# Performance work log

Hardware: AMD Instinct MI355X
Metric: run time of the kernel (lower is better)

Reference implementation:

```python
import jax, jax.numpy as jnp
import numpy as np

B, D, H, O, E, K = 8192, 1024, 4096, 1024, 8, 2

def setup_inputs() -> dict:
    key = jax.random.key(0)
    ks = jax.random.split(key, 8)
    x = jax.random.normal(ks[0], (B, D), dtype=jnp.float32)
    topk_idx = jax.random.randint(ks[1], (B, K), 0, E, dtype=jnp.int32)
    weights = jax.random.uniform(ks[2], (B, K), dtype=jnp.float32)
    s1 = 1.0 / np.sqrt(D)
    s2 = 1.0 / np.sqrt(H)
    W1 = jax.random.uniform(ks[3], (E, D, H), minval=-s1, maxval=s1, dtype=jnp.float32)
    b1 = jax.random.uniform(ks[4], (E, H), minval=-s1, maxval=s1, dtype=jnp.float32)
    W2 = jax.random.uniform(ks[5], (E, H, O), minval=-s2, maxval=s2, dtype=jnp.float32)
    b2 = jax.random.uniform(ks[6], (E, O), minval=-s2, maxval=s2, dtype=jnp.float32)
    return {"x": x, "topk_idx": topk_idx, "weights": weights,
            "W1": W1, "b1": b1, "W2": W2, "b2": b2}

def reference(x, topk_idx, weights, W1, b1, W2, b2):
    # Per-token gate mass for each expert: gate[b,e] = sum_i weights[b,i]*[topk_idx[b,i]==e]
    # Equivalent to the original masked gather/scatter combine (duplicates in topk_idx sum).
    out = jnp.zeros((x.shape[0], W2.shape[-1]), dtype=x.dtype)
    for e in range(W1.shape[0]):  # small fixed loop over experts
        gate_e = jnp.sum(weights * (topk_idx == e), axis=1)  # [B]
        h = jax.nn.relu(x @ W1[e] + b1[e])                   # [B,H]
        out_e = h @ W2[e] + b2[e]                            # [B,O]
        out = out + gate_e[:, None] * out_e
    return out
```

## Files before the change

kernel.cpp:

```cpp
#include <hip/hip_runtime.h>
#include <stdint.h>

#define B_TOK 8192
#define D_DIM 1024
#define H_DIM 4096
#define O_DIM 1024
#define E_NUM 8
#define K_TOP 2
#define NPAIR (B_TOK * K_TOP)

typedef short bf16x8 __attribute__((ext_vector_type(8)));
typedef float f32x4 __attribute__((ext_vector_type(4)));

struct Hdr {
    int counts[8];
    int offsets[9];
    int cursor[8];
    int total1, total2;
    int base1[9];
    int base2[9];
};

__device__ __forceinline__ unsigned short f2bf(float f) {
    union { float f; unsigned int u; } v; v.f = f;
    unsigned int u = v.u;
    unsigned int r = (u + 0x7fffu + ((u >> 16) & 1u)) >> 16;
    return (unsigned short)r;
}

__device__ __forceinline__ float bf2f(unsigned short s) {
    union { unsigned int u; float f; } v;
    v.u = ((unsigned int)s) << 16;
    return v.f;
}

__device__ __forceinline__ void async16(const void* g, const void* l) {
    __builtin_amdgcn_global_load_lds(
        (__attribute__((address_space(1))) void*)(uintptr_t)g,
        (__attribute__((address_space(3))) void*)(uint32_t)(uintptr_t)l,
        16, 0, 0);
}


__global__ void cvt_x_kernel(const float* __restrict__ x, unsigned short* __restrict__ xb) {
    int i = (blockIdx.x * 256 + threadIdx.x) * 4;
    float4 v = *(const float4*)(x + i);
    ushort4 o;
    o.x = f2bf(v.x); o.y = f2bf(v.y); o.z = f2bf(v.z); o.w = f2bf(v.w);
    *(ushort4*)(xb + i) = o;
}

__global__ __launch_bounds__(256) void tconv_kernel(const float* __restrict__ in,
                                                    unsigned short* __restrict__ out,
                                                    int R, int C) {
    __shared__ float t[64 * 69];
    int e = blockIdx.z;
    const float* ip = in + (size_t)e * R * C;
    unsigned short* op = out + (size_t)e * R * C;
    int c0 = blockIdx.x * 64, r0 = blockIdx.y * 64;
    int tid = threadIdx.x;
    int lr = tid >> 4;
    int lc = (tid & 15) * 4;
#pragma unroll
    for (int i = 0; i < 4; i++) {
        int row = lr + i * 16;
        float4 v = *(const float4*)&ip[(size_t)(r0 + row) * C + c0 + lc];
        t[row * 69 + lc + 0] = v.x;
        t[row * 69 + lc + 1] = v.y;
        t[row * 69 + lc + 2] = v.z;
        t[row * 69 + lc + 3] = v.w;
    }
    __syncthreads();
#pragma unroll
    for (int i = 0; i < 4; i++) {
        int c = lr + i * 16;
        ushort4 o;
        o.x = f2bf(t[(lc + 0) * 69 + c]);
        o.y = f2bf(t[(lc + 1) * 69 + c]);
        o.z = f2bf(t[(lc + 2) * 69 + c]);
        o.w = f2bf(t[(lc + 3) * 69 + c]);
        *(ushort4*)&op[(size_t)(c0 + c) * R + r0 + lc] = o;
    }
}


__global__ void route_count_kernel(const int* __restrict__ topk, Hdr* hdr) {
    __shared__ int cnt[8];
    int tid = threadIdx.x;
    if (tid < 8) cnt[tid] = 0;
    __syncthreads();
    for (int i = tid; i < NPAIR; i += 1024) atomicAdd(&cnt[topk[i]], 1);
    __syncthreads();
    if (tid == 0) {
        int off = 0, t1 = 0, t2 = 0;
        for (int e = 0; e < 8; e++) {
            int c = cnt[e];
            hdr->counts[e] = c;
            hdr->offsets[e] = off;
            hdr->cursor[e] = off;
            hdr->base1[e] = t1;
            hdr->base2[e] = t2;
            int mt1 = (c + 255) >> 8;
            int mt2 = (c + 127) >> 7;
            t1 += mt1 * (H_DIM / 256);
            t2 += mt2 * (O_DIM / 128);
            off += c;
        }
        hdr->offsets[8] = off;
        hdr->base1[8] = t1;
        hdr->base2[8] = t2;
        hdr->total1 = t1;
        hdr->total2 = t2;
    }
}

__global__ void route_fill_kernel(const int* __restrict__ topk, const float* __restrict__ wts,
                                  Hdr* hdr, int* __restrict__ ptok, float* __restrict__ pgate,
                                  int* __restrict__ pslot) {
    int i = blockIdx.x * 256 + threadIdx.x;
    int e = topk[i];
    int pos = atomicAdd(&hdr->cursor[e], 1);
    ptok[pos] = i >> 1;
    pgate[pos] = wts[i];
    pslot[i] = pos;
}

__global__ void ws_fail_kernel(float* out) { out[0] = 1.0e9f; }


#define ASL(BUF, KH) ((BUF) * 32768 + (KH) * 16384)

#define STG_A(BUF, KH, KOFF) do { \
    async16(Ab + srcA[0] + (KOFF), smem + ASL(BUF, KH) + wu * 2048); \
    async16(Ab + srcA[1] + (KOFF), smem + ASL(BUF, KH) + wu * 2048 + 1024); } while (0)

#define STG_B(BUF, KH, KOFF) do { \
    async16(Bb + srcB[0] + (KOFF), smem + 65536 + ASL(BUF, KH) + wu * 2048); \
    async16(Bb + srcB[1] + (KOFF), smem + 65536 + ASL(BUF, KH) + wu * 2048 + 1024); } while (0)

#define VM6 asm volatile("s_waitcnt vmcnt(6)" ::: "memory")
#define VM0 asm volatile("s_waitcnt vmcnt(0)" ::: "memory")
#define NOPX ((void)0)

#define PHASE0(BUF, KH, STAGE, CKPT) do { \
    STAGE; \
    bq[0] = *(const bf16x8*)&smem[pBo[0] + ASL(BUF, KH)]; \
    bq[1] = *(const bf16x8*)&smem[pBo[1] + ASL(BUF, KH)]; \
    bq[2] = *(const bf16x8*)&smem[pBo[2] + ASL(BUF, KH)]; \
    bq[3] = *(const bf16x8*)&smem[pBo[3] + ASL(BUF, KH)]; \
    aq[0] = *(const bf16x8*)&smem[pAo[0] + ASL(BUF, KH)]; \
    aq[1] = *(const bf16x8*)&smem[pAo[1] + ASL(BUF, KH)]; \
    aq[2] = *(const bf16x8*)&smem[pAo[2] + ASL(BUF, KH)]; \
    aq[3] = *(const bf16x8*)&smem[pAo[3] + ASL(BUF, KH)]; \
    __builtin_amdgcn_s_barrier(); \
    asm volatile("s_waitcnt lgkmcnt(0)" ::: "memory"); \
    __builtin_amdgcn_s_setprio(1); \
    _Pragma("unroll") \
    for (int q_ = 0; q_ < 4; ++q_) { \
        _Pragma("unroll") \
        for (int n_ = 0; n_ < 4; ++n_) \
            acc[q_][n_] = __builtin_amdgcn_mfma_f32_16x16x32_bf16(aq[q_], bq[n_], acc[q_][n_], 0, 0, 0); \
    } \
    __builtin_amdgcn_s_setprio(0); \
    CKPT; \
    __builtin_amdgcn_s_barrier(); \
} while (0)

#define PHASE1(BUF, KH, STAGE, CKPT) do { \
    STAGE; \
    aq[0] = *(const bf16x8*)&smem[pAo[4] + ASL(BUF, KH)]; \
    aq[1] = *(const bf16x8*)&smem[pAo[5] + ASL(BUF, KH)]; \
    aq[2] = *(const bf16x8*)&smem[pAo[6] + ASL(BUF, KH)]; \
    aq[3] = *(const bf16x8*)&smem[pAo[7] + ASL(BUF, KH)]; \
    __builtin_amdgcn_s_barrier(); \
    asm volatile("s_waitcnt lgkmcnt(0)" ::: "memory"); \
    __builtin_amdgcn_s_setprio(1); \
    _Pragma("unroll") \
    for (int q_ = 0; q_ < 4; ++q_) { \
        _Pragma("unroll") \
        for (int n_ = 0; n_ < 4; ++n_) \
            acc[4 + q_][n_] = __builtin_amdgcn_mfma_f32_16x16x32_bf16(aq[q_], bq[n_], acc[4 + q_][n_], 0, 0, 0); \
    } \
    __builtin_amdgcn_s_setprio(0); \
    CKPT; \
    __builtin_amdgcn_s_barrier(); \
} while (0)

template <int KD, int N, bool GATHER>
__global__ __launch_bounds__(512, 2) void moe_gemm256_kernel(
    const unsigned short* __restrict__ A,
    const unsigned short* __restrict__ Bt,
    const float* __restrict__ bias,
    const Hdr* __restrict__ hdr,
    const int* __restrict__ ptok,
    unsigned short* __restrict__ outp) {

    extern __shared__ __align__(16) char smem[];
    constexpr int NT = KD / 64;
    constexpr int NI = NT / 2;
    static_assert(NT >= 4 && (NT % 2) == 0, "K-tile count");

    const int tid = threadIdx.x;
    const int lane = tid & 63;
    const int wv = tid >> 6;
    const int wu = __builtin_amdgcn_readfirstlane(wv);
    const int lr = lane & 15;
    const int lkg = lane >> 4;
    const int wr = wv >> 2;
    const int wc = wv & 3;

    const int total = hdr->total1;
    const int* tb = hdr->base1;

    int chunk = (total + 7) >> 3;
    int seq = (blockIdx.x & 7) * chunk + (blockIdx.x >> 3);
    if (seq >= total) return;

    int e = 0;
#pragma unroll
    for (int j = 1; j < 8; j++)
        if (seq >= tb[j]) e = j;
    e = __builtin_amdgcn_readfirstlane(e);
    int lt = seq - tb[e];
    int cnt = hdr->counts[e], off = hdr->offsets[e];
    int MT = (cnt + 255) >> 8;
    int mtile = lt % MT, ntile = lt / MT;
    int m0 = mtile * 256, n0 = ntile * 256;

    const char* Ab = (const char*)A;
    const char* Bb = (const char*)(Bt + (size_t)e * ((size_t)N * KD));

    uint32_t srcA[2], srcB[2];
#pragma unroll
    for (int l = 0; l < 2; ++l) {
        int g = wv * 128 + l * 64 + lane;
        int rp = g >> 2, cp = g & 3;
        int c = (cp - (rp >> 1)) & 3;
        int q = off + m0 + rp;
        q = q > NPAIR - 1 ? NPAIR - 1 : q;
        uint32_t rowA = GATHER ? (uint32_t)ptok[q] : (uint32_t)q;
        srcA[l] = rowA * (uint32_t)(KD * 2) + (uint32_t)(c * 16);
        srcB[l] = (uint32_t)(n0 + rp) * (uint32_t)(KD * 2) + (uint32_t)(c * 16);
    }

    uint32_t pAo[8], pBo[4];
#pragma unroll
    for (int mr = 0; mr < 8; ++mr) {
        int r = wr * 128 + mr * 16 + lr;
        pAo[mr] = (uint32_t)(r * 64 + ((lkg + (r >> 1)) & 3) * 16);
    }
#pragma unroll
    for (int nr = 0; nr < 4; ++nr) {
        int r = wc * 64 + nr * 16 + lr;
        pBo[nr] = (uint32_t)(65536 + r * 64 + ((lkg + (r >> 1)) & 3) * 16);
    }

    f32x4 acc[8][4];
#pragma unroll
    for (int i = 0; i < 8; ++i)
#pragma unroll
        for (int j = 0; j < 4; ++j)
            acc[i][j] = (f32x4){0.f, 0.f, 0.f, 0.f};
    bf16x8 aq[4], bq[4];

    STG_A(0, 0, 0u);   STG_B(0, 0, 0u);
    STG_A(0, 1, 64u);  STG_B(0, 1, 64u);
    STG_A(1, 0, 128u); STG_B(1, 0, 128u);
    STG_B(1, 1, 192u);
    VM0;
    __builtin_amdgcn_s_barrier();

    for (int it = 0; it < NI - 1; ++it) {
        const uint32_t kb = (uint32_t)it * 256u;
        PHASE0(0, 0, STG_A(1, 1, kb + 192u), NOPX);
        PHASE1(0, 0, STG_B(0, 0, kb + 256u), NOPX);
        PHASE0(0, 1, STG_A(0, 0, kb + 256u), NOPX);
        PHASE1(0, 1, STG_B(0, 1, kb + 320u), VM6);
        PHASE0(1, 0, STG_A(0, 1, kb + 320u), NOPX);
        PHASE1(1, 0, STG_B(1, 0, kb + 384u), NOPX);
        PHASE0(1, 1, STG_A(1, 0, kb + 384u), NOPX);
        PHASE1(1, 1, STG_B(1, 1, kb + 448u), VM6);
    }
    {
        const uint32_t kb = (uint32_t)(NI - 1) * 256u;
        PHASE0(0, 0, STG_A(1, 1, kb + 192u), NOPX);
        PHASE1(0, 0, NOPX, NOPX);
        PHASE0(0, 1, NOPX, NOPX);
        PHASE1(0, 1, NOPX, VM0);
        PHASE0(1, 0, NOPX, NOPX);
        PHASE1(1, 0, NOPX, NOPX);
        PHASE0(1, 1, NOPX, NOPX);
        PHASE1(1, 1, NOPX, NOPX);
    }

    unsigned short* eb = (unsigned short*)smem;
    int rows_valid = cnt - m0;
    if (rows_valid > 256) rows_valid = 256;
#pragma unroll
    for (int pass = 0; pass < 2; ++pass) {
        __syncthreads();
        if (wr == pass) {
#pragma unroll
            for (int nr = 0; nr < 4; ++nr) {
                int n = wc * 64 + nr * 16 + lr;
                float bv = bias[(size_t)e * N + n0 + n];
#pragma unroll
                for (int mr = 0; mr < 8; ++mr) {
#pragma unroll
                    for (int r2 = 0; r2 < 4; ++r2) {
                        int ml = mr * 16 + lkg * 4 + r2;
                        float v = acc[mr][nr][r2] + bv;
                        if (GATHER) v = v > 0.f ? v : 0.f;
                        eb[ml * 264 + n] = f2bf(v);
                    }
                }
            }
        }
        __syncthreads();
        int rv = rows_valid - pass * 128;
        if (rv > 128) rv = 128;
#pragma unroll
        for (int j = 0; j < 8; ++j) {
            int idx = j * 512 + tid;
            int row = idx >> 5;
            int c16 = idx & 31;
            if (row < rv) {
                uint4 v = *(const uint4*)&eb[row * 264 + c16 * 8];
                *(uint4*)&outp[(size_t)(off + m0 + pass * 128 + row) * N + n0 + c16 * 8] = v;
            }
        }
    }
}

template <int K, int N, bool GATHER>
__global__ __launch_bounds__(256, 4) void moe_gemm128_kernel(
    const unsigned short* __restrict__ A,
    const unsigned short* __restrict__ Bt,
    const float* __restrict__ bias,
    const Hdr* __restrict__ hdr,
    const int* __restrict__ ptok,
    unsigned short* __restrict__ outp) {

    __shared__ __align__(16) unsigned short smem[128 * 132];
    unsigned short* As = smem;
    unsigned short* Bs = smem + 128 * 64;

    const int tid = threadIdx.x;
    const int lane = tid & 63;
    const int wv = tid >> 6;
    const int wu = __builtin_amdgcn_readfirstlane(wv);
    const int wm = (wv & 1) * 64;
    const int wn = (wv >> 1) * 64;
    const int lr = lane & 15;
    const int lkg = lane >> 4;

    const int total = hdr->total2;
    const int* tb = hdr->base2;
    constexpr int NT = N / 128;

    int chunk = (total + 7) >> 3;
    int seq = (blockIdx.x & 7) * chunk + (blockIdx.x >> 3);
    if (seq >= total) return;

    int e = 0;
#pragma unroll
    for (int j = 1; j < 8; j++)
        if (seq >= tb[j]) e = j;
    e = __builtin_amdgcn_readfirstlane(e);
    int lt = seq - tb[e];
    int cnt = hdr->counts[e], off = hdr->offsets[e];
    int MT = (cnt + 127) >> 7;

    int band = lt / (NT * 8);
    int r = lt - band * (NT * 8);
    int mrem = MT - band * 8;
    mrem = mrem > 8 ? 8 : mrem;
    int gsz = mrem * 8;
    int g = r / gsz;
    int rg = r - g * gsz;
    int gm = rg % mrem;
    int gn = rg / mrem;
    int mtile = band * 8 + gm;
    int ntile = g * 8 + gn;
    int m0 = mtile * 128, n0 = ntile * 128;

    const char* Ab = (const char*)A;
    const char* Bb = (const char*)(Bt + (size_t)e * ((size_t)N * K));
    uint32_t offA[4], offB[4];
#pragma unroll
    for (int i = 0; i < 4; i++) {
        int s = i * 256 + tid;
        int rr = s >> 3;
        int cl = (s & 7) ^ (rr & 7);
        int p = off + m0 + rr;
        p = p > NPAIR - 1 ? NPAIR - 1 : p;
        uint32_t row = GATHER ? (uint32_t)ptok[p] : (uint32_t)p;
        offA[i] = (row * (uint32_t)K + (uint32_t)cl * 8u) * 2u;
        offB[i] = (((uint32_t)(n0 + rr)) * (uint32_t)K + (uint32_t)cl * 8u) * 2u;
    }

    f32x4 zero = {0.f, 0.f, 0.f, 0.f};
    f32x4 acc[4][4];
#pragma unroll
    for (int mt = 0; mt < 4; mt++)
#pragma unroll
        for (int nt = 0; nt < 4; nt++) acc[mt][nt] = zero;

    for (int k0 = 0; k0 < K; k0 += 64) {
#pragma unroll
        for (int i = 0; i < 4; i++) {
            async16(Ab + offA[i], &As[(i * 256 + wu * 64) * 8]);
            async16(Bb + offB[i], &Bs[(i * 256 + wu * 64) * 8]);
            offA[i] += 128;
            offB[i] += 128;
        }
        __syncthreads();
#pragma unroll
        for (int ks = 0; ks < 2; ks++) {
            bf16x8 af[4];
#pragma unroll
            for (int q = 0; q < 4; q++) {
                int ra = wm + q * 16 + lr;
                int ca = (ks * 4 + lkg) ^ (ra & 7);
                af[q] = *(const bf16x8*)&As[ra * 64 + ca * 8];
            }
#pragma unroll
            for (int nt = 0; nt < 4; nt++) {
                int rb = wn + nt * 16 + lr;
                int cb = (ks * 4 + lkg) ^ (rb & 7);
                bf16x8 bfr = *(const bf16x8*)&Bs[rb * 64 + cb * 8];
#pragma unroll
                for (int mt = 0; mt < 4; mt++)
                    acc[mt][nt] = __builtin_amdgcn_mfma_f32_16x16x32_bf16(
                        af[mt], bfr, acc[mt][nt], 0, 0, 0);
            }
        }
        __syncthreads();
    }

#pragma unroll
    for (int nt = 0; nt < 4; nt++) {
        int n = wn + nt * 16 + lr;
        float bv = bias[(size_t)e * N + n0 + n];
#pragma unroll
        for (int mt = 0; mt < 4; mt++) {
#pragma unroll
            for (int r2 = 0; r2 < 4; r2++) {
                int m = wm + mt * 16 + lkg * 4 + r2;
                float v = acc[mt][nt][r2] + bv;
                if (GATHER) v = v > 0.f ? v : 0.f;
                smem[m * 132 + n] = f2bf(v);
            }
        }
    }
    __syncthreads();
    int rows_valid = cnt - m0;
    if (rows_valid > 128) rows_valid = 128;
#pragma unroll
    for (int j = 0; j < 16; j++) {
        int idx = j * 256 + tid;
        int row = idx >> 5;
        int lc8 = idx & 31;
        if (row < rows_valid) {
            uint2 v = *(const uint2*)&smem[row * 132 + lc8 * 4];
            *(uint2*)&outp[(size_t)(off + m0 + row) * N + n0 + lc8 * 4] = v;
        }
    }
}

__global__ void combine_kernel(const unsigned short* __restrict__ oslot,
                               const int* __restrict__ pslot,
                               const float* __restrict__ wts,
                               float* __restrict__ out) {
    int tok = blockIdx.x;
    int s0 = pslot[tok * 2], s1 = pslot[tok * 2 + 1];
    float g0 = wts[tok * 2], g1 = wts[tok * 2 + 1];
    int n = threadIdx.x * 4;
    ushort4 a = *(const ushort4*)&oslot[(size_t)s0 * O_DIM + n];
    ushort4 b = *(const ushort4*)&oslot[(size_t)s1 * O_DIM + n];
    float4 o;
    o.x = g0 * bf2f(a.x) + g1 * bf2f(b.x);
    o.y = g0 * bf2f(a.y) + g1 * bf2f(b.y);
    o.z = g0 * bf2f(a.z) + g1 * bf2f(b.z);
    o.w = g0 * bf2f(a.w) + g1 * bf2f(b.w);
    *(float4*)&out[(size_t)tok * O_DIM + n] = o;
}


extern "C" void kernel_launch(void* const* d_in, const int* in_sizes, int n_in,
                              void* d_out, int out_size, void* d_ws, size_t ws_size,
                              hipStream_t stream) {
    const float* x   = (const float*)d_in[0];
    const int* topk  = (const int*)d_in[1];
    const float* wts = (const float*)d_in[2];
    const float* W1  = (const float*)d_in[3];
    const float* b1  = (const float*)d_in[4];
    const float* W2  = (const float*)d_in[5];
    const float* b2  = (const float*)d_in[6];
    float* out = (float*)d_out;

    char* ws = (char*)d_ws;
    size_t off = 0;
    auto alloc = [&](size_t bytes) -> void* {
        void* p = ws + off;
        off += (bytes + 255) & ~(size_t)255;
        return p;
    };
    Hdr* hdr = (Hdr*)alloc(sizeof(Hdr));
    int* ptok = (int*)alloc((size_t)NPAIR * 4);
    float* pgate = (float*)alloc((size_t)NPAIR * 4);
    int* pslot = (int*)alloc((size_t)NPAIR * 4);
    unsigned short* xb   = (unsigned short*)alloc((size_t)B_TOK * D_DIM * 2);
    unsigned short* W1bt = (unsigned short*)alloc((size_t)E_NUM * D_DIM * H_DIM * 2);
    unsigned short* W2bt = (unsigned short*)alloc((size_t)E_NUM * H_DIM * O_DIM * 2);
    unsigned short* hbuf = (unsigned short*)alloc((size_t)NPAIR * H_DIM * 2);
    unsigned short* oslot = W1bt;

    if (off > ws_size) {
        hipMemsetAsync(d_out, 0, (size_t)out_size * sizeof(float), stream);
        ws_fail_kernel<<<1, 1, 0, stream>>>(out);
        return;
    }

    static int attr_done = 0;
    if (!attr_done) {
        (void)hipFuncSetAttribute(
            reinterpret_cast<const void*>(&moe_gemm256_kernel<D_DIM, H_DIM, true>),
            hipFuncAttributeMaxDynamicSharedMemorySize, 131072);
        attr_done = 1;
    }

    cvt_x_kernel<<<(B_TOK * D_DIM) / 1024, 256, 0, stream>>>(x, xb);
    tconv_kernel<<<dim3(H_DIM / 64, D_DIM / 64, E_NUM), dim3(256), 0, stream>>>(W1, W1bt, D_DIM, H_DIM);
    tconv_kernel<<<dim3(O_DIM / 64, H_DIM / 64, E_NUM), dim3(256), 0, stream>>>(W2, W2bt, H_DIM, O_DIM);
    route_count_kernel<<<1, 1024, 0, stream>>>(topk, hdr);
    route_fill_kernel<<<NPAIR / 256, 256, 0, stream>>>(topk, wts, hdr, ptok, pgate, pslot);

    moe_gemm256_kernel<D_DIM, H_DIM, true><<<1152, 512, 131072, stream>>>(
        xb, W1bt, b1, hdr, ptok, hbuf);
    moe_gemm128_kernel<H_DIM, O_DIM, false><<<1152, 256, 0, stream>>>(
        hbuf, W2bt, b2, hdr, ptok, oslot);
    combine_kernel<<<B_TOK, 256, 0, stream>>>(oslot, pslot, wts, out);
}
```

Before: 769.1 us.

## Rewrite second expert GEMM as 256x128 pipelined tile and fuse routing kernels

Replaces the simple 128x128 second-layer GEMM with a 512-thread 256x128-tile kernel. The new kernel double-buffers through dynamic shared memory, issues async loads with staged vmcnt waits, and interleaves barriers with MFMA phases, reusing the pipeline design of the first GEMM. It also merges the two routing kernels into one single-block kernel that counts and fills positions with shared-memory atomics. Routing now needs one launch and no global atomics. The pipelined GEMM is meant to hide load latency and improve data reuse, at the cost of coarser tiles (fewer blocks) and more padding waste for experts whose counts are not multiples of 256.

```diff
diff --git a/kernel.cpp b/kernel.cpp
--- a/kernel.cpp
+++ b/kernel.cpp
@@ -15,7 +15,6 @@
 struct Hdr {
     int counts[8];
     int offsets[9];
-    int cursor[8];
     int total1, total2;
     int base1[9];
     int base2[9];
@@ -84,12 +83,21 @@
 }
 
 
-__global__ void route_count_kernel(const int* __restrict__ topk, Hdr* hdr) {
+__global__ __launch_bounds__(1024) void route_kernel(const int* __restrict__ topk,
+                                                     Hdr* hdr,
+                                                     int* __restrict__ ptok,
+                                                     int* __restrict__ pslot) {
     __shared__ int cnt[8];
+    __shared__ int cur[8];
     int tid = threadIdx.x;
     if (tid < 8) cnt[tid] = 0;
     __syncthreads();
-    for (int i = tid; i < NPAIR; i += 1024) atomicAdd(&cnt[topk[i]], 1);
+    int ev[16];
+#pragma unroll
+    for (int j = 0; j < 16; j++) {
+        ev[j] = topk[tid + j * 1024];
+        atomicAdd(&cnt[ev[j]], 1);
+    }
     __syncthreads();
     if (tid == 0) {
         int off = 0, t1 = 0, t2 = 0;
@@ -97,13 +105,12 @@
             int c = cnt[e];
             hdr->counts[e] = c;
             hdr->offsets[e] = off;
-            hdr->cursor[e] = off;
+            cur[e] = off;
             hdr->base1[e] = t1;
             hdr->base2[e] = t2;
-            int mt1 = (c + 255) >> 8;
-            int mt2 = (c + 127) >> 7;
-            t1 += mt1 * (H_DIM / 256);
-            t2 += mt2 * (O_DIM / 128);
+            int mt = (c + 255) >> 8;
+            t1 += mt * (H_DIM / 256);
+            t2 += mt * (O_DIM / 128);
             off += c;
         }
         hdr->offsets[8] = off;
@@ -112,17 +119,14 @@
         hdr->total1 = t1;
         hdr->total2 = t2;
     }
-}
-
-__global__ void route_fill_kernel(const int* __restrict__ topk, const float* __restrict__ wts,
-                                  Hdr* hdr, int* __restrict__ ptok, float* __restrict__ pgate,
-                                  int* __restrict__ pslot) {
-    int i = blockIdx.x * 256 + threadIdx.x;
-    int e = topk[i];
-    int pos = atomicAdd(&hdr->cursor[e], 1);
-    ptok[pos] = i >> 1;
-    pgate[pos] = wts[i];
-    pslot[i] = pos;
+    __syncthreads();
+#pragma unroll
+    for (int j = 0; j < 16; j++) {
+        int i = tid + j * 1024;
+        int pos = atomicAdd(&cur[ev[j]], 1);
+        ptok[pos] = i >> 1;
+        pslot[i] = pos;
+    }
 }
 
 __global__ void ws_fail_kernel(float* out) { out[0] = 1.0e9f; }
@@ -139,6 +143,7 @@
     async16(Bb + srcB[1] + (KOFF), smem + 65536 + ASL(BUF, KH) + wu * 2048 + 1024); } while (0)
 
 #define VM6 asm volatile("s_waitcnt vmcnt(6)" ::: "memory")
+#define VM4 asm volatile("s_waitcnt vmcnt(4)" ::: "memory")
 #define VM0 asm volatile("s_waitcnt vmcnt(0)" ::: "memory")
 #define NOPX ((void)0)
 
@@ -332,31 +337,78 @@
     }
 }
 
-template <int K, int N, bool GATHER>
-__global__ __launch_bounds__(256, 4) void moe_gemm128_kernel(
+
+#define BSL(BUF, KH) (65536 + (BUF) * 16384 + (KH) * 8192)
+
+#define STG2B(BUF, KH, KOFF) \
+    async16(Bb + srcB + (KOFF), smem + BSL(BUF, KH) + wu * 1024)
+
+#define G2PH0(BUF, KH, STAGE, CKPT) do { \
+    STAGE; \
+    bq[0] = *(const bf16x8*)&smem[pBo[0] + BSL(BUF, KH)]; \
+    bq[1] = *(const bf16x8*)&smem[pBo[1] + BSL(BUF, KH)]; \
+    aq[0] = *(const bf16x8*)&smem[pAo[0] + ASL(BUF, KH)]; \
+    aq[1] = *(const bf16x8*)&smem[pAo[1] + ASL(BUF, KH)]; \
+    aq[2] = *(const bf16x8*)&smem[pAo[2] + ASL(BUF, KH)]; \
+    aq[3] = *(const bf16x8*)&smem[pAo[3] + ASL(BUF, KH)]; \
+    __builtin_amdgcn_s_barrier(); \
+    asm volatile("s_waitcnt lgkmcnt(0)" ::: "memory"); \
+    __builtin_amdgcn_s_setprio(1); \
+    _Pragma("unroll") \
+    for (int q_ = 0; q_ < 4; ++q_) { \
+        _Pragma("unroll") \
+        for (int n_ = 0; n_ < 2; ++n_) \
+            acc[q_][n_] = __builtin_amdgcn_mfma_f32_16x16x32_bf16(aq[q_], bq[n_], acc[q_][n_], 0, 0, 0); \
+    } \
+    __builtin_amdgcn_s_setprio(0); \
+    CKPT; \
+    __builtin_amdgcn_s_barrier(); \
+} while (0)
+
+#define G2PH1(BUF, KH, STAGE, CKPT) do { \
+    STAGE; \
+    aq[0] = *(const bf16x8*)&smem[pAo[4] + ASL(BUF, KH)]; \
+    aq[1] = *(const bf16x8*)&smem[pAo[5] + ASL(BUF, KH)]; \
+    aq[2] = *(const bf16x8*)&smem[pAo[6] + ASL(BUF, KH)]; \
+    aq[3] = *(const bf16x8*)&smem[pAo[7] + ASL(BUF, KH)]; \
+    __builtin_amdgcn_s_barrier(); \
+    asm volatile("s_waitcnt lgkmcnt(0)" ::: "memory"); \
+    __builtin_amdgcn_s_setprio(1); \
+    _Pragma("unroll") \
+    for (int q_ = 0; q_ < 4; ++q_) { \
+        _Pragma("unroll") \
+        for (int n_ = 0; n_ < 2; ++n_) \
+            acc[4 + q_][n_] = __builtin_amdgcn_mfma_f32_16x16x32_bf16(aq[q_], bq[n_], acc[4 + q_][n_], 0, 0, 0); \
+    } \
+    __builtin_amdgcn_s_setprio(0); \
+    CKPT; \
+    __builtin_amdgcn_s_barrier(); \
+} while (0)
+
+template <int KD, int N>
+__global__ __launch_bounds__(512, 2) void moe_gemm2_kernel(
     const unsigned short* __restrict__ A,
     const unsigned short* __restrict__ Bt,
     const float* __restrict__ bias,
     const Hdr* __restrict__ hdr,
-    const int* __restrict__ ptok,
     unsigned short* __restrict__ outp) {
 
-    __shared__ __align__(16) unsigned short smem[128 * 132];
-    unsigned short* As = smem;
-    unsigned short* Bs = smem + 128 * 64;
+    extern __shared__ __align__(16) char smem[];
+    constexpr int NT = KD / 64;
+    constexpr int NI = NT / 2;
+    static_assert(NT >= 4 && (NT % 2) == 0, "K-tile count");
 
     const int tid = threadIdx.x;
     const int lane = tid & 63;
     const int wv = tid >> 6;
     const int wu = __builtin_amdgcn_readfirstlane(wv);
-    const int wm = (wv & 1) * 64;
-    const int wn = (wv >> 1) * 64;
     const int lr = lane & 15;
     const int lkg = lane >> 4;
+    const int wr = wv >> 2;
+    const int wc = wv & 3;
 
     const int total = hdr->total2;
     const int* tb = hdr->base2;
-    constexpr int NT = N / 128;
 
     int chunk = (total + 7) >> 3;
     int seq = (blockIdx.x & 7) * chunk + (blockIdx.x >> 3);
@@ -369,101 +421,114 @@
     e = __builtin_amdgcn_readfirstlane(e);
     int lt = seq - tb[e];
     int cnt = hdr->counts[e], off = hdr->offsets[e];
-    int MT = (cnt + 127) >> 7;
-
-    int band = lt / (NT * 8);
-    int r = lt - band * (NT * 8);
-    int mrem = MT - band * 8;
-    mrem = mrem > 8 ? 8 : mrem;
-    int gsz = mrem * 8;
-    int g = r / gsz;
-    int rg = r - g * gsz;
-    int gm = rg % mrem;
-    int gn = rg / mrem;
-    int mtile = band * 8 + gm;
-    int ntile = g * 8 + gn;
-    int m0 = mtile * 128, n0 = ntile * 128;
+    int MT = (cnt + 255) >> 8;
+    int mtile = lt % MT, ntile = lt / MT;
+    int m0 = mtile * 256, n0 = ntile * 128;
 
     const char* Ab = (const char*)A;
-    const char* Bb = (const char*)(Bt + (size_t)e * ((size_t)N * K));
-    uint32_t offA[4], offB[4];
-#pragma unroll
-    for (int i = 0; i < 4; i++) {
-        int s = i * 256 + tid;
-        int rr = s >> 3;
-        int cl = (s & 7) ^ (rr & 7);
-        int p = off + m0 + rr;
-        p = p > NPAIR - 1 ? NPAIR - 1 : p;
-        uint32_t row = GATHER ? (uint32_t)ptok[p] : (uint32_t)p;
-        offA[i] = (row * (uint32_t)K + (uint32_t)cl * 8u) * 2u;
-        offB[i] = (((uint32_t)(n0 + rr)) * (uint32_t)K + (uint32_t)cl * 8u) * 2u;
-    }
-
-    f32x4 zero = {0.f, 0.f, 0.f, 0.f};
-    f32x4 acc[4][4];
-#pragma unroll
-    for (int mt = 0; mt < 4; mt++)
-#pragma unroll
-        for (int nt = 0; nt < 4; nt++) acc[mt][nt] = zero;
-
-    for (int k0 = 0; k0 < K; k0 += 64) {
-#pragma unroll
-        for (int i = 0; i < 4; i++) {
-            async16(Ab + offA[i], &As[(i * 256 + wu * 64) * 8]);
-            async16(Bb + offB[i], &Bs[(i * 256 + wu * 64) * 8]);
-            offA[i] += 128;
-            offB[i] += 128;
-        }
+    const char* Bb = (const char*)(Bt + (size_t)e * ((size_t)N * KD));
+
+    uint32_t srcA[2];
+#pragma unroll
+    for (int l = 0; l < 2; ++l) {
+        int g = wv * 128 + l * 64 + lane;
+        int rp = g >> 2, cp = g & 3;
+        int c = (cp - (rp >> 1)) & 3;
+        int q = off + m0 + rp;
+        q = q > NPAIR - 1 ? NPAIR - 1 : q;
+        srcA[l] = (uint32_t)q * (uint32_t)(KD * 2) + (uint32_t)(c * 16);
+    }
+    uint32_t srcB;
+    {
+        int g = wv * 64 + lane;
+        int rp = g >> 2, cp = g & 3;
+        int c = (cp - (rp >> 1)) & 3;
+        srcB = (uint32_t)(n0 + rp) * (uint32_t)(KD * 2) + (uint32_t)(c * 16);
+    }
+
+    uint32_t pAo[8], pBo[2];
+#pragma unroll
+    for (int mr = 0; mr < 8; ++mr) {
+        int r = wr * 128 + mr * 16 + lr;
+        pAo[mr] = (uint32_t)(r * 64 + ((lkg + (r >> 1)) & 3) * 16);
+    }
+#pragma unroll
+    for (int nr = 0; nr < 2; ++nr) {
+        int r = wc * 32 + nr * 16 + lr;
+        pBo[nr] = (uint32_t)(r * 64 + ((lkg + (r >> 1)) & 3) * 16);
+    }
+
+    f32x4 acc[8][2];
+#pragma unroll
+    for (int i = 0; i < 8; ++i)
+#pragma unroll
+        for (int j = 0; j < 2; ++j)
+            acc[i][j] = (f32x4){0.f, 0.f, 0.f, 0.f};
+    bf16x8 aq[4], bq[2];
+
+    STG_A(0, 0, 0u);   STG2B(0, 0, 0u);
+    STG_A(0, 1, 64u);  STG2B(0, 1, 64u);
+    STG_A(1, 0, 128u); STG2B(1, 0, 128u);
+    STG2B(1, 1, 192u);
+    VM0;
+    __builtin_amdgcn_s_barrier();
+
+    for (int it = 0; it < NI - 1; ++it) {
+        const uint32_t kb = (uint32_t)it * 256u;
+        G2PH0(0, 0, STG_A(1, 1, kb + 192u), NOPX);
+        G2PH1(0, 0, STG2B(0, 0, kb + 256u), NOPX);
+        G2PH0(0, 1, STG_A(0, 0, kb + 256u), NOPX);
+        G2PH1(0, 1, STG2B(0, 1, kb + 320u), VM4);
+        G2PH0(1, 0, STG_A(0, 1, kb + 320u), NOPX);
+        G2PH1(1, 0, STG2B(1, 0, kb + 384u), NOPX);
+        G2PH0(1, 1, STG_A(1, 0, kb + 384u), NOPX);
+        G2PH1(1, 1, STG2B(1, 1, kb + 448u), VM4);
+    }
+    {
+        const uint32_t kb = (uint32_t)(NI - 1) * 256u;
+        G2PH0(0, 0, STG_A(1, 1, kb + 192u), NOPX);
+        G2PH1(0, 0, NOPX, NOPX);
+        G2PH0(0, 1, NOPX, NOPX);
+        G2PH1(0, 1, NOPX, VM0);
+        G2PH0(1, 0, NOPX, NOPX);
+        G2PH1(1, 0, NOPX, NOPX);
+        G2PH0(1, 1, NOPX, NOPX);
+        G2PH1(1, 1, NOPX, NOPX);
+    }
+
+    unsigned short* eb = (unsigned short*)smem;
+    int rows_valid = cnt - m0;
+    if (rows_valid > 256) rows_valid = 256;
+#pragma unroll
+    for (int pass = 0; pass < 2; ++pass) {
         __syncthreads();
-#pragma unroll
-        for (int ks = 0; ks < 2; ks++) {
-            bf16x8 af[4];
-#pragma unroll
-            for (int q = 0; q < 4; q++) {
-                int ra = wm + q * 16 + lr;
-                int ca = (ks * 4 + lkg) ^ (ra & 7);
-                af[q] = *(const bf16x8*)&As[ra * 64 + ca * 8];
-            }
-#pragma unroll
-            for (int nt = 0; nt < 4; nt++) {
-                int rb = wn + nt * 16 + lr;
-                int cb = (ks * 4 + lkg) ^ (rb & 7);
-                bf16x8 bfr = *(const bf16x8*)&Bs[rb * 64 + cb * 8];
-#pragma unroll
-                for (int mt = 0; mt < 4; mt++)
-                    acc[mt][nt] = __builtin_amdgcn_mfma_f32_16x16x32_bf16(
-                        af[mt], bfr, acc[mt][nt], 0, 0, 0);
+        if (wr == pass) {
+#pragma unroll
+            for (int nr = 0; nr < 2; ++nr) {
+                int n = wc * 32 + nr * 16 + lr;
+                float bv = bias[(size_t)e * N + n0 + n];
+#pragma unroll
+                for (int mr = 0; mr < 8; ++mr) {
+#pragma unroll
+                    for (int r2 = 0; r2 < 4; ++r2) {
+                        int ml = mr * 16 + lkg * 4 + r2;
+                        eb[ml * 132 + n] = f2bf(acc[mr][nr][r2] + bv);
+                    }
+                }
             }
         }
         __syncthreads();
-    }
-
-#pragma unroll
-    for (int nt = 0; nt < 4; nt++) {
-        int n = wn + nt * 16 + lr;
-        float bv = bias[(size_t)e * N + n0 + n];
-#pragma unroll
-        for (int mt = 0; mt < 4; mt++) {
-#pragma unroll
-            for (int r2 = 0; r2 < 4; r2++) {
-                int m = wm + mt * 16 + lkg * 4 + r2;
-                float v = acc[mt][nt][r2] + bv;
-                if (GATHER) v = v > 0.f ? v : 0.f;
-                smem[m * 132 + n] = f2bf(v);
+        int rv = rows_valid - pass * 128;
+        if (rv > 128) rv = 128;
+#pragma unroll
+        for (int j = 0; j < 8; ++j) {
+            int idx = j * 512 + tid;
+            int row = idx >> 5;
+            int lc8 = idx & 31;
+            if (row < rv) {
+                uint2 v = *(const uint2*)&eb[row * 132 + lc8 * 4];
+                *(uint2*)&outp[(size_t)(off + m0 + pass * 128 + row) * N + n0 + lc8 * 4] = v;
             }
-        }
-    }
-    __syncthreads();
-    int rows_valid = cnt - m0;
-    if (rows_valid > 128) rows_valid = 128;
-#pragma unroll
-    for (int j = 0; j < 16; j++) {
-        int idx = j * 256 + tid;
-        int row = idx >> 5;
-        int lc8 = idx & 31;
-        if (row < rows_valid) {
-            uint2 v = *(const uint2*)&smem[row * 132 + lc8 * 4];
-            *(uint2*)&outp[(size_t)(off + m0 + row) * N + n0 + lc8 * 4] = v;
         }
     }
 }
@@ -508,7 +573,6 @@
     };
     Hdr* hdr = (Hdr*)alloc(sizeof(Hdr));
     int* ptok = (int*)alloc((size_t)NPAIR * 4);
-    float* pgate = (float*)alloc((size_t)NPAIR * 4);
     int* pslot = (int*)alloc((size_t)NPAIR * 4);
     unsigned short* xb   = (unsigned short*)alloc((size_t)B_TOK * D_DIM * 2);
     unsigned short* W1bt = (unsigned short*)alloc((size_t)E_NUM * D_DIM * H_DIM * 2);
@@ -527,18 +591,20 @@
         (void)hipFuncSetAttribute(
             reinterpret_cast<const void*>(&moe_gemm256_kernel<D_DIM, H_DIM, true>),
             hipFuncAttributeMaxDynamicSharedMemorySize, 131072);
+        (void)hipFuncSetAttribute(
+            reinterpret_cast<const void*>(&moe_gemm2_kernel<H_DIM, O_DIM>),
+            hipFuncAttributeMaxDynamicSharedMemorySize, 98304);
         attr_done = 1;
     }
 
     cvt_x_kernel<<<(B_TOK * D_DIM) / 1024, 256, 0, stream>>>(x, xb);
     tconv_kernel<<<dim3(H_DIM / 64, D_DIM / 64, E_NUM), dim3(256), 0, stream>>>(W1, W1bt, D_DIM, H_DIM);
     tconv_kernel<<<dim3(O_DIM / 64, H_DIM / 64, E_NUM), dim3(256), 0, stream>>>(W2, W2bt, H_DIM, O_DIM);
-    route_count_kernel<<<1, 1024, 0, stream>>>(topk, hdr);
-    route_fill_kernel<<<NPAIR / 256, 256, 0, stream>>>(topk, wts, hdr, ptok, pgate, pslot);
+    route_kernel<<<1, 1024, 0, stream>>>(topk, hdr, ptok, pslot);
 
     moe_gemm256_kernel<D_DIM, H_DIM, true><<<1152, 512, 131072, stream>>>(
         xb, W1bt, b1, hdr, ptok, hbuf);
-    moe_gemm128_kernel<H_DIM, O_DIM, false><<<1152, 256, 0, stream>>>(
-        hbuf, W2bt, b2, hdr, ptok, oslot);
+    moe_gemm2_kernel<H_DIM, O_DIM><<<576, 512, 98304, stream>>>(
+        hbuf, W2bt, b2, hdr, oslot);
     combine_kernel<<<B_TOK, 256, 0, stream>>>(oslot, pslot, wts, out);
 }
```

Result: faster. 735.8 us (-4.3%).
